# Optimization experiments

Measured on AMD Instinct MI355X. Metric: run time of the kernel, lower is better.

## Reference

```python
import jax, jax.numpy as jnp
import numpy as np

N_NODES = 20000
N_EDGES = 160000
N_CONFIG = 1000
OP_SIZE = 120
OP_FEATURE = 140
CONFIG_FEATURE = 24
HID = 256
EMB = 128


def _mynorm(x, axis):
    # InstanceNorm1d (affine=False): biased var, eps=1e-5, normalized over `axis`
    m = jnp.mean(x, axis=axis, keepdims=True)
    v = jnp.var(x, axis=axis, keepdims=True)
    return (x - m) / jnp.sqrt(v + 1e-5)


def _gelu(x):
    return jax.nn.gelu(x, approximate=False)


def _segment_softmax(e, seg, num):
    m = jax.ops.segment_max(e, seg, num_segments=num)
    ex = jnp.exp(e - m[seg])
    s = jax.ops.segment_sum(ex, seg, num_segments=num)
    return ex / (s[seg] + 1e-16)


def setup_inputs() -> dict:
    key = jax.random.key(0)
    ks = jax.random.split(key, 24)
    d = {}
    d['node_feat'] = jax.random.normal(ks[0], (N_NODES, OP_FEATURE), jnp.float32)
    d['config_feat'] = jax.random.normal(ks[1], (N_CONFIG, CONFIG_FEATURE), jnp.float32)
    d['node_feat_mean'] = jax.random.normal(ks[2], (OP_FEATURE,), jnp.float32)
    d['node_feat_std'] = jax.random.uniform(ks[3], (OP_FEATURE,), jnp.float32)
    d['config_feat_mean'] = jax.random.normal(ks[4], (CONFIG_FEATURE,), jnp.float32)
    d['config_feat_std'] = jax.random.uniform(ks[5], (CONFIG_FEATURE,), jnp.float32)
    d['embed_table'] = jax.random.normal(ks[6], (OP_SIZE, EMB), jnp.float32)
    d['early_W1'] = jax.random.normal(ks[7], (EMB + OP_FEATURE, HID), jnp.float32) * 0.05
    d['early_W2'] = jax.random.normal(ks[8], (HID, HID), jnp.float32) * 0.05
    d['gat_Wl'] = jax.random.normal(ks[9], (4, HID, HID), jnp.float32) * 0.05
    d['gat_bl'] = jax.random.normal(ks[10], (4, HID), jnp.float32) * 0.05
    d['gat_Wr'] = jax.random.normal(ks[11], (4, HID, HID), jnp.float32) * 0.05
    d['gat_br'] = jax.random.normal(ks[12], (4, HID), jnp.float32) * 0.05
    d['gat_att'] = jax.random.normal(ks[13], (4, HID), jnp.float32) * 0.05
    d['gat_bias'] = jax.random.normal(ks[14], (4, HID), jnp.float32) * 0.05
    d['late_W1'] = jax.random.normal(ks[15], (HID + CONFIG_FEATURE, HID), jnp.float32) * 0.05
    d['late_W2'] = jax.random.normal(ks[16], (HID, HID // 2), jnp.float32) * 0.05
    d['pred_W'] = jax.random.normal(ks[17], (HID // 2, 1), jnp.float32) * 0.05
    d['pred_b'] = jax.random.normal(ks[18], (1,), jnp.float32) * 0.05
    d['node_opcode'] = jax.random.randint(ks[19], (N_NODES,), 0, OP_SIZE, jnp.int64)
    d['edge_index'] = jax.random.randint(ks[20], (2, N_EDGES), 0, N_NODES, jnp.int64)
    return d


def reference(node_feat, config_feat, node_feat_mean, node_feat_std,
              config_feat_mean, config_feat_std, embed_table,
              early_W1, early_W2, gat_Wl, gat_bl, gat_Wr, gat_br,
              gat_att, gat_bias, late_W1, late_W2, pred_W, pred_b,
              node_opcode, edge_index):
    N = node_feat.shape[0]
    # embedding with max_norm=1: renormalize looked-up rows to L2 norm <= 1
    emb = embed_table[node_opcode]
    nrm = jnp.sqrt(jnp.sum(emb * emb, axis=-1, keepdims=True))
    emb = emb * jnp.minimum(1.0, 1.0 / (nrm + 1e-7))
    feat = (node_feat - node_feat_mean) / (node_feat_std + 1e-4)
    x = jnp.concatenate([emb, feat], axis=-1)  # [N, 268]
    # early MLP (norm over node axis per channel)
    x = _gelu(_mynorm(x @ early_W1, 0))
    x = _gelu(_mynorm(x @ early_W2, 0))
    # add self loops (PyG GATv2Conv default)
    loop = jnp.arange(N, dtype=edge_index.dtype)
    src = jnp.concatenate([edge_index[0], loop])  # message source j
    dst = jnp.concatenate([edge_index[1], loop])  # message target i
    for i in range(4):
        xl = x @ gat_Wl[i] + gat_bl[i]
        xr = x @ gat_Wr[i] + gat_br[i]
        h = xl[src] + xr[dst]                      # [E+N, HID]
        e = jax.nn.leaky_relu(h, 0.2) @ gat_att[i]  # [E+N]
        alpha = _segment_softmax(e, dst, N)
        out = jax.ops.segment_sum(alpha[:, None] * xl[src], dst, num_segments=N)
        out = out + gat_bias[i]
        x = _gelu(_mynorm(out, 0))
    pool = jnp.mean(x, axis=0) + jnp.max(x, axis=0)  # [HID]
    cf = (config_feat - config_feat_mean) / (config_feat_std + 1e-4)
    C = cf.shape[0]
    x_late = jnp.concatenate([cf, jnp.broadcast_to(pool, (C, pool.shape[0]))], axis=1)
    h = _gelu(_mynorm(x_late @ late_W1, 0))  # 2D MyNorm1d normalizes over batch axis
    h = _gelu(_mynorm(h @ late_W2, 0))
    runtime = (h @ pred_W + pred_b)[:, 0]
    return runtime
```

## Files before the change

### kernel.cpp

```cpp
#include <hip/hip_runtime.h>
#include <math.h>

#define N_NODES 20000
#define N_EDGES 160000
#define N_CFG   1000
#define OP_FEAT 140
#define CFG_FEAT 24
#define HID     256
#define EMB     128
#define E_TOT   (N_EDGES + N_NODES)
#define K288    288
#define MPAD    20096
#define NW      512

typedef __attribute__((ext_vector_type(8))) short short8v;
typedef __attribute__((ext_vector_type(4))) float f32x4;

__device__ __forceinline__ short f2bf(float f) {
  unsigned u = __float_as_uint(f);
  unsigned r = (u + 0x7FFFu + ((u >> 16) & 1u)) >> 16;
  return (short)r;
}
__device__ __forceinline__ float bf2f(short s) {
  return __uint_as_float(((unsigned)(unsigned short)s) << 16);
}
__device__ __forceinline__ float gelu_f(float x) {
  return 0.5f * x * (1.0f + erff(x * 0.70710678118654752f));
}

#define GLOAD_LDS(gptr, lptr) __builtin_amdgcn_global_load_lds( \
    (const __attribute__((address_space(1))) void*)(gptr),      \
    (__attribute__((address_space(3))) void*)(lptr), 16, 0, 0)

__global__ void prep_weights(
    const float* __restrict__ eW1, const float* __restrict__ eW2,
    const float* __restrict__ lW1, const float* __restrict__ lW2,
    const float* __restrict__ Wl, const float* __restrict__ Wr,
    const float* __restrict__ bl, const float* __restrict__ br,
    short* __restrict__ W1t, short* __restrict__ W2t,
    short* __restrict__ lW1t, short* __restrict__ lW2t,
    short* __restrict__ Wlrt, float* __restrict__ blr)
{
  int i = blockIdx.x * 256 + threadIdx.x;
  const int s1 = HID * K288;
  const int s2 = HID * HID;
  const int s3 = HID * K288;
  const int s4 = 128 * HID;
  const int s5 = 4 * NW * HID;
  const int s6 = 4 * NW;
  if (i < s1) { int n = i / K288, k = i % K288;
    W1t[i] = (k < EMB + OP_FEAT) ? f2bf(eW1[(size_t)k * HID + n]) : (short)0; return; }
  i -= s1;
  if (i < s2) { int n = i >> 8, k = i & 255;
    W2t[i] = f2bf(eW2[(size_t)k * HID + n]); return; }
  i -= s2;
  if (i < s3) { int n = i / K288, k = i % K288;
    lW1t[i] = (k < CFG_FEAT + HID) ? f2bf(lW1[(size_t)k * HID + n]) : (short)0; return; }
  i -= s3;
  if (i < s4) { int n = i >> 8, k = i & 255;
    lW2t[i] = f2bf(lW2[(size_t)k * 128 + n]); return; }
  i -= s4;
  if (i < s5) { int l = i >> 17, rem = i & 131071, n = rem >> 8, k = rem & 255;
    float v = (n < HID) ? Wl[(size_t)l * HID * HID + (size_t)k * HID + n]
                        : Wr[(size_t)l * HID * HID + (size_t)k * HID + (n - HID)];
    Wlrt[i] = f2bf(v); return; }
  i -= s5;
  if (i < s6) { int l = i >> 9, j = i & 511;
    blr[i] = (j < HID) ? bl[l * HID + j] : br[l * HID + j - HID]; }
}

__global__ __launch_bounds__(256) void prep_kernel(
    const float* __restrict__ node_feat, const float* __restrict__ nf_mean,
    const float* __restrict__ nf_std, const float* __restrict__ emb_table,
    const int* __restrict__ opcode, short* __restrict__ x268b)
{
  int wave = threadIdx.x >> 6;
  int lane = threadIdx.x & 63;
  int row = blockIdx.x * 4 + wave;
  if (row >= N_NODES) return;
  int op = opcode[row];
  float t0 = emb_table[op * EMB + lane];
  float t1 = emb_table[op * EMB + 64 + lane];
  float ss = t0 * t0 + t1 * t1;
  #pragma unroll
  for (int off = 32; off; off >>= 1) ss += __shfl_xor(ss, off);
  float sc = fminf(1.0f, 1.0f / (sqrtf(ss) + 1e-7f));
  short* dst = x268b + (size_t)row * K288;
  dst[lane] = f2bf(t0 * sc);
  dst[64 + lane] = f2bf(t1 * sc);
  for (int k = lane; k < OP_FEAT; k += 64)
    dst[EMB + k] = f2bf((node_feat[(size_t)row * OP_FEAT + k] - nf_mean[k]) / (nf_std[k] + 1e-4f));
  if (lane < K288 - EMB - OP_FEAT) dst[EMB + OP_FEAT + lane] = 0;
}

template<int BM, int BN>
__global__ __launch_bounds__(256) void gemm_mfma(
    const short* __restrict__ A, const short* __restrict__ Wt,
    const float* __restrict__ bias, float* __restrict__ C,
    short* __restrict__ Cb, float* __restrict__ stats,
    int M, int N, int Kpad)
{
  constexpr int MI = (BM == 128) ? 4 : 2;
  constexpr int NI = (BN == 128) ? 4 : 2;
  __shared__ __align__(16) short As[2][4][BM][8];
  __shared__ __align__(16) short Bs[2][4][BN][8];
  int tid = threadIdx.x;
  int wave = tid >> 6, lane = tid & 63;
  int bm = blockIdx.x * BM, bn = blockIdx.y * BN;
  int wr = (BM == 128) ? (wave >> 1) * 64 : (wave >> 1) * 32;
  int wc = (BM == 128) ? (wave & 1) * 64 : (wave & 1) * 32;
  int g = lane >> 4, r16 = lane & 15;
  f32x4 acc[MI][NI] = {};
  int nt = Kpad >> 5;

  auto STAGE = [&](int t, int b) {
    int k0 = t * 32;
    if constexpr (BM == 128) {
      #pragma unroll
      for (int s2 = 0; s2 < 2; s2++) {
        int s = wave * 2 + s2;
        int sg = s >> 1, r0 = (s & 1) * 64;
        GLOAD_LDS(A  + (size_t)(bm + r0 + lane) * Kpad + k0 + sg * 8, &As[b][sg][r0][0]);
        GLOAD_LDS(Wt + (size_t)(bn + r0 + lane) * Kpad + k0 + sg * 8, &Bs[b][sg][r0][0]);
      }
    } else {
      GLOAD_LDS(A  + (size_t)(bm + lane) * Kpad + k0 + wave * 8, &As[b][wave][0][0]);
      GLOAD_LDS(Wt + (size_t)(bn + lane) * Kpad + k0 + wave * 8, &Bs[b][wave][0][0]);
    }
  };

  STAGE(0, 0);
  for (int t = 0; t < nt; t++) {
    int b = t & 1;
    __syncthreads();
    if (t + 1 < nt) STAGE(t + 1, b ^ 1);
    short8v af[MI], bfv[NI];
    #pragma unroll
    for (int mi = 0; mi < MI; mi++)
      af[mi] = *(const short8v*)&As[b][g][wr + mi * 16 + r16][0];
    #pragma unroll
    for (int ni = 0; ni < NI; ni++)
      bfv[ni] = *(const short8v*)&Bs[b][g][wc + ni * 16 + r16][0];
    #pragma unroll
    for (int mi = 0; mi < MI; mi++)
      #pragma unroll
      for (int ni = 0; ni < NI; ni++)
        acc[mi][ni] = __builtin_amdgcn_mfma_f32_16x16x32_bf16(af[mi], bfv[ni], acc[mi][ni], 0, 0, 0);
  }

  int rg = lane >> 4;
  #pragma unroll
  for (int ni = 0; ni < NI; ni++) {
    int gc = bn + wc + ni * 16 + r16;
    float bv = bias ? bias[gc] : 0.f;
    float s = 0.f, sq = 0.f;
    #pragma unroll
    for (int mi = 0; mi < MI; mi++) {
      #pragma unroll
      for (int r = 0; r < 4; r++) {
        int gr = bm + wr + mi * 16 + rg * 4 + r;
        if (gr < M) {
          float v = acc[mi][ni][r] + bv;
          if (C)  C[(size_t)gr * N + gc] = v;
          if (Cb) Cb[(size_t)gr * N + gc] = f2bf(v);
          s += v; sq += v * v;
        }
      }
    }
    if (stats) {
      s  += __shfl_xor(s, 16);  sq += __shfl_xor(sq, 16);
      s  += __shfl_xor(s, 32);  sq += __shfl_xor(sq, 32);
      if (rg == 0) { atomicAdd(&stats[gc], s); atomicAdd(&stats[N + gc], sq); }
    }
  }
}

__global__ void colstats(const float* __restrict__ X, int M, int C,
                         float* __restrict__ stats)
{
  int c = threadIdx.x;
  int r0 = blockIdx.x * 64;
  int r1 = min(r0 + 64, M);
  float s = 0.f, sq = 0.f;
  for (int r = r0; r < r1; r++) {
    float v = X[(size_t)r * C + c];
    s += v; sq += v * v;
  }
  atomicAdd(&stats[c], s);
  atomicAdd(&stats[C + c], sq);
}

__global__ void norm_gelu_col(const float* __restrict__ X, short* __restrict__ Yb,
                              int M, int C, const float* __restrict__ stats,
                              float* __restrict__ psum, unsigned* __restrict__ pmax)
{
  int c = threadIdx.x;
  int r0 = blockIdx.x * 32, r1 = min(r0 + 32, M);
  float invM = 1.0f / (float)M;
  float mean = stats[c] * invM;
  float var = stats[C + c] * invM - mean * mean;
  float inv = rsqrtf(var + 1e-5f);
  float s = 0.f, mx = -INFINITY;
  for (int r = r0; r < r1; r++) {
    float y = gelu_f((X[(size_t)r * C + c] - mean) * inv);
    Yb[(size_t)r * C + c] = f2bf(y);
    s += y; mx = fmaxf(mx, y);
  }
  if (psum) {
    unsigned b = __float_as_uint(mx);
    unsigned enc = (b & 0x80000000u) ? ~b : (b | 0x80000000u);
    atomicAdd(&psum[c], s);
    atomicMax(&pmax[c], enc);
  }
}

__global__ void edge_count(const int* __restrict__ ei, int* __restrict__ counts) {
  int e = blockIdx.x * blockDim.x + threadIdx.x;
  if (e >= E_TOT) return;
  int dst = (e < N_EDGES) ? ei[N_EDGES + e] : (e - N_EDGES);
  atomicAdd(&counts[dst], 1);
}

__global__ __launch_bounds__(1024) void scan_kernel(const int* __restrict__ counts,
                                                    int* __restrict__ indptr)
{
  __shared__ int sh[1024];
  int t = threadIdx.x;
  const int chunk = (N_NODES + 1023) / 1024;
  int start = t * chunk, end = min(start + chunk, N_NODES);
  int sum = 0;
  for (int i = start; i < end; i++) sum += counts[i];
  sh[t] = sum;
  __syncthreads();
  for (int off = 1; off < 1024; off <<= 1) {
    int v = (t >= off) ? sh[t - off] : 0;
    __syncthreads();
    sh[t] += v;
    __syncthreads();
  }
  int run = (t > 0) ? sh[t - 1] : 0;
  for (int i = start; i < end; i++) { indptr[i] = run; run += counts[i]; }
  if (t == 1023) indptr[N_NODES] = run;
}

__global__ void edge_fill(const int* __restrict__ ei, const int* __restrict__ indptr,
                          int* __restrict__ cursor, int* __restrict__ col)
{
  int e = blockIdx.x * blockDim.x + threadIdx.x;
  if (e >= E_TOT) return;
  int src, dst;
  if (e < N_EDGES) { src = ei[e]; dst = ei[N_EDGES + e]; }
  else             { src = dst = e - N_EDGES; }
  int pos = indptr[dst] + atomicAdd(&cursor[dst], 1);
  col[pos] = src;
}

__global__ __launch_bounds__(256) void gat_agg(
    const short* __restrict__ xlr,
    const int* __restrict__ indptr, const int* __restrict__ col,
    const float* __restrict__ att, const float* __restrict__ bias,
    float* __restrict__ out)
{
  int wave = threadIdx.x >> 6, lane = threadIdx.x & 63;
  int node = blockIdx.x * 4 + wave;
  if (node >= N_NODES) return;
  float attc[4], xri[4], o[4] = {0, 0, 0, 0};
  {
    short4 xr4 = *(const short4*)(xlr + (size_t)node * NW + HID + lane * 4);
    #pragma unroll
    for (int k = 0; k < 4; k++) {
      attc[k] = att[lane * 4 + k];
      xri[k] = bf2f(((short*)&xr4)[k]);
    }
  }
  float m = -INFINITY, s = 0.f;
  int e0 = indptr[node], e1 = indptr[node + 1];
  for (int e = e0; e < e1; e += 4) {
    float p[4];
    float xlj[4][4];
    #pragma unroll
    for (int b = 0; b < 4; b++) {
      bool valid = (e + b) < e1;
      int j = col[valid ? e + b : e0];
      short4 xl4 = *(const short4*)(xlr + (size_t)j * NW + lane * 4);
      float pp = 0.f;
      #pragma unroll
      for (int k = 0; k < 4; k++) {
        xlj[b][k] = bf2f(((short*)&xl4)[k]);
        float h = xlj[b][k] + xri[k];
        float lr = h > 0.f ? h : 0.2f * h;
        pp += lr * attc[k];
      }
      p[b] = valid ? pp : -INFINITY;
    }
    #pragma unroll
    for (int off = 32; off; off >>= 1) {
      #pragma unroll
      for (int b = 0; b < 4; b++) p[b] += __shfl_xor(p[b], off);
    }
    float mn = fmaxf(m, fmaxf(fmaxf(p[0], p[1]), fmaxf(p[2], p[3])));
    float scale = __expf(m - mn);
    float w[4];
    #pragma unroll
    for (int b = 0; b < 4; b++) w[b] = __expf(p[b] - mn);
    s = s * scale + w[0] + w[1] + w[2] + w[3];
    #pragma unroll
    for (int k = 0; k < 4; k++)
      o[k] = o[k] * scale + w[0] * xlj[0][k] + w[1] * xlj[1][k]
                          + w[2] * xlj[2][k] + w[3] * xlj[3][k];
    m = mn;
  }
  float inv = 1.0f / (s + 1e-16f);
  f32x4 ov;
  #pragma unroll
  for (int k = 0; k < 4; k++) ov[k] = o[k] * inv + bias[lane * 4 + k];
  *(f32x4*)(out + (size_t)node * HID + lane * 4) = ov;
}

__device__ __forceinline__ float fdec(unsigned u) {
  unsigned b = (u & 0x80000000u) ? (u & 0x7FFFFFFFu) : ~u;
  return __uint_as_float(b);
}

__global__ void build_xlate(const float* __restrict__ cfg, const float* __restrict__ cmean,
                            const float* __restrict__ cstd, const float* __restrict__ psum,
                            const unsigned* __restrict__ pmax, short* __restrict__ xlateb)
{
  int i = blockIdx.x * blockDim.x + threadIdx.x;
  if (i >= N_CFG * K288) return;
  int r = i / K288, c = i % K288;
  float v;
  if (c < CFG_FEAT) v = (cfg[r * CFG_FEAT + c] - cmean[c]) / (cstd[c] + 1e-4f);
  else if (c < CFG_FEAT + HID) {
    int p = c - CFG_FEAT;
    v = psum[p] * (1.0f / N_NODES) + fdec(pmax[p]);
  } else v = 0.f;
  xlateb[i] = f2bf(v);
}

__global__ __launch_bounds__(64) void pred_kernel(
    const float* __restrict__ h2, const float* __restrict__ stats,
    const float* __restrict__ W, const float* __restrict__ b,
    float* __restrict__ out)
{
  int r = blockIdx.x, lane = threadIdx.x;
  const float invM = 1.0f / (float)N_CFG;
  float v = 0.f;
  #pragma unroll
  for (int t = 0; t < 2; t++) {
    int c = lane + 64 * t;
    float mean = stats[c] * invM;
    float var = stats[128 + c] * invM - mean * mean;
    float y = gelu_f((h2[(size_t)r * 128 + c] - mean) * rsqrtf(var + 1e-5f));
    v += y * W[c];
  }
  #pragma unroll
  for (int off = 32; off; off >>= 1) v += __shfl_xor(v, off);
  if (lane == 0) out[r] = v + b[0];
}

extern "C" void kernel_launch(void* const* d_in, const int* in_sizes, int n_in,
                              void* d_out, int out_size, void* d_ws, size_t ws_size,
                              hipStream_t stream)
{
  const float* node_feat   = (const float*)d_in[0];
  const float* config_feat = (const float*)d_in[1];
  const float* nf_mean     = (const float*)d_in[2];
  const float* nf_std      = (const float*)d_in[3];
  const float* cf_mean     = (const float*)d_in[4];
  const float* cf_std      = (const float*)d_in[5];
  const float* emb_table   = (const float*)d_in[6];
  const float* early_W1    = (const float*)d_in[7];
  const float* early_W2    = (const float*)d_in[8];
  const float* gat_Wl      = (const float*)d_in[9];
  const float* gat_bl      = (const float*)d_in[10];
  const float* gat_Wr      = (const float*)d_in[11];
  const float* gat_br      = (const float*)d_in[12];
  const float* gat_att     = (const float*)d_in[13];
  const float* gat_bias    = (const float*)d_in[14];
  const float* late_W1     = (const float*)d_in[15];
  const float* late_W2     = (const float*)d_in[16];
  const float* pred_W      = (const float*)d_in[17];
  const float* pred_b      = (const float*)d_in[18];
  const int*   node_opcode = (const int*)d_in[19];
  const int*   edge_index  = (const int*)d_in[20];
  float* out = (float*)d_out;
  (void)in_sizes; (void)n_in; (void)out_size; (void)ws_size;

  char* ws = (char*)d_ws;
  size_t off = 0;
  auto alloc = [&](size_t bytes) -> void* {
    void* p = ws + off;
    off += (bytes + 255) & ~255ull;
    return p;
  };
  short* x268b = (short*)alloc((size_t)MPAD * K288 * 2);
  float* bufB  = (float*)alloc((size_t)N_NODES * HID * 4);
  short* bufAb = (short*)alloc((size_t)MPAD * HID * 2);
  short* xlr   = (short*)alloc((size_t)N_NODES * NW * 2);
  int* indptr  = (int*)alloc((N_NODES + 1) * 4);
  int* colidx  = (int*)alloc((size_t)E_TOT * 4);
  short* xlateb = (short*)alloc((size_t)1024 * K288 * 2);
  float* h1    = (float*)alloc((size_t)N_CFG * HID * 4);
  short* h1b   = (short*)alloc((size_t)1024 * HID * 2);
  float* h2    = (float*)alloc((size_t)N_CFG * 128 * 4);
  short* W1t   = (short*)alloc((size_t)HID * K288 * 2);
  short* W2t   = (short*)alloc((size_t)HID * HID * 2);
  short* Wlrt  = (short*)alloc((size_t)4 * NW * HID * 2);
  float* blr   = (float*)alloc(4 * NW * 4);
  short* lW1t  = (short*)alloc((size_t)HID * K288 * 2);
  short* lW2t  = (short*)alloc((size_t)128 * HID * 2);

  float* zbase = (float*)alloc((8 * 1024 + 512 + 2 * N_NODES) * 4);
  float* stats8 = zbase;
  float* psum   = zbase + 8192;
  unsigned* pmax = (unsigned*)(zbase + 8192 + 256);
  int* counts   = (int*)(zbase + 8192 + 512);
  int* cursor   = counts + N_NODES;
  const size_t zbytes = (8 * 1024 + 512 + 2 * N_NODES) * 4;
  auto slot = [&](int s) { return stats8 + s * 1024; };

  auto run_gemm = [&](int BM, const short* A, const short* Wt, const float* bias, float* C,
                      short* Cb, float* stats, int M, int N, int Kpad) {
    if (BM == 128) {
      dim3 grid((M + 127) / 128, N / 128);
      hipLaunchKernelGGL((gemm_mfma<128, 128>), grid, dim3(256), 0, stream,
                         A, Wt, bias, C, Cb, stats, M, N, Kpad);
    } else {
      dim3 grid((M + 63) / 64, N / 64);
      hipLaunchKernelGGL((gemm_mfma<64, 64>), grid, dim3(256), 0, stream,
                         A, Wt, bias, C, Cb, stats, M, N, Kpad);
    }
  };
  auto run_norm = [&](const float* X, short* Yb, int M, int C, float* stats,
                      float* ps, unsigned* pm) {
    hipLaunchKernelGGL(norm_gelu_col, dim3((M + 31) / 32), dim3(C), 0, stream,
                       X, Yb, M, C, stats, ps, pm);
  };

  hipMemsetAsync(zbase, 0, zbytes, stream);

  {
    int total = HID * K288 + HID * HID + HID * K288 + 128 * HID + 4 * NW * HID + 4 * NW;
    hipLaunchKernelGGL(prep_weights, dim3((total + 255) / 256), dim3(256), 0, stream,
                       early_W1, early_W2, late_W1, late_W2, gat_Wl, gat_Wr, gat_bl, gat_br,
                       W1t, W2t, lW1t, lW2t, Wlrt, blr);
  }

  hipLaunchKernelGGL(edge_count, dim3((E_TOT + 255) / 256), dim3(256), 0, stream,
                     edge_index, counts);
  hipLaunchKernelGGL(scan_kernel, dim3(1), dim3(1024), 0, stream, counts, indptr);
  hipLaunchKernelGGL(edge_fill, dim3((E_TOT + 255) / 256), dim3(256), 0, stream,
                     edge_index, indptr, cursor, colidx);

  hipLaunchKernelGGL(prep_kernel, dim3((N_NODES + 3) / 4), dim3(256), 0, stream,
                     node_feat, nf_mean, nf_std, emb_table, node_opcode, x268b);
  run_gemm(64, x268b, W1t, nullptr, bufB, nullptr, slot(0), N_NODES, HID, K288);
  run_norm(bufB, bufAb, N_NODES, HID, slot(0), nullptr, nullptr);
  run_gemm(64, bufAb, W2t, nullptr, bufB, nullptr, slot(1), N_NODES, HID, HID);
  run_norm(bufB, bufAb, N_NODES, HID, slot(1), nullptr, nullptr);

  for (int l = 0; l < 4; l++) {
    run_gemm(128, bufAb, Wlrt + (size_t)l * NW * HID, blr + l * NW, nullptr, xlr, nullptr,
             N_NODES, NW, HID);
    hipLaunchKernelGGL(gat_agg, dim3((N_NODES + 3) / 4), dim3(256), 0, stream,
                       xlr, indptr, colidx, gat_att + l * HID, gat_bias + l * HID, bufB);
    hipLaunchKernelGGL(colstats, dim3((N_NODES + 63) / 64), dim3(HID), 0, stream,
                       bufB, N_NODES, HID, slot(2 + l));
    run_norm(bufB, bufAb, N_NODES, HID, slot(2 + l),
             (l == 3) ? psum : nullptr, (l == 3) ? pmax : nullptr);
  }

  hipLaunchKernelGGL(build_xlate, dim3((N_CFG * K288 + 255) / 256), dim3(256), 0, stream,
                     config_feat, cf_mean, cf_std, psum, pmax, xlateb);
  run_gemm(64, xlateb, lW1t, nullptr, h1, nullptr, slot(6), N_CFG, HID, K288);
  run_norm(h1, h1b, N_CFG, HID, slot(6), nullptr, nullptr);
  run_gemm(64, h1b, lW2t, nullptr, h2, nullptr, slot(7), N_CFG, 128, HID);
  hipLaunchKernelGGL(pred_kernel, dim3(N_CFG), dim3(64), 0, stream,
                     h2, slot(7), pred_W, pred_b, out);
}
```

Measured before the change: 560.7 us.

## Fuse column statistics into GAT aggregation and process two nodes per wave

Removes the separate colstats pass by accumulating per-column sum and sum-of-squares in shared memory inside gat_agg and flushing them with one global atomic per column per block. Each wave now handles two destination nodes, with 32 lanes per node doing 8-wide bf16 loads, which halves the shuffle reduction depth and widens memory accesses. The two half-waves iterate to the larger of the two degrees, so uneven degrees waste some work. Shared-memory atomics add contention in exchange for skipping a full re-read of the 20000x256 fp32 output.

Result: slower. 726.2 us (+29.5%).

```diff
diff --git a/kernel.cpp b/kernel.cpp
--- a/kernel.cpp
+++ b/kernel.cpp
@@ -175,21 +175,6 @@
   }
 }
 
-__global__ void colstats(const float* __restrict__ X, int M, int C,
-                         float* __restrict__ stats)
-{
-  int c = threadIdx.x;
-  int r0 = blockIdx.x * 64;
-  int r1 = min(r0 + 64, M);
-  float s = 0.f, sq = 0.f;
-  for (int r = r0; r < r1; r++) {
-    float v = X[(size_t)r * C + c];
-    s += v; sq += v * v;
-  }
-  atomicAdd(&stats[c], s);
-  atomicAdd(&stats[C + c], sq);
-}
-
 __global__ void norm_gelu_col(const float* __restrict__ X, short* __restrict__ Yb,
                               int M, int C, const float* __restrict__ stats,
                               float* __restrict__ psum, unsigned* __restrict__ pmax)
@@ -259,34 +244,43 @@
     const short* __restrict__ xlr,
     const int* __restrict__ indptr, const int* __restrict__ col,
     const float* __restrict__ att, const float* __restrict__ bias,
-    float* __restrict__ out)
-{
-  int wave = threadIdx.x >> 6, lane = threadIdx.x & 63;
-  int node = blockIdx.x * 4 + wave;
-  if (node >= N_NODES) return;
-  float attc[4], xri[4], o[4] = {0, 0, 0, 0};
+    float* __restrict__ out, float* __restrict__ stats)
+{
+  __shared__ float sums[HID];
+  __shared__ float sqs[HID];
+  int tid = threadIdx.x;
+  if (tid < HID) { sums[tid] = 0.f; sqs[tid] = 0.f; }
+  __syncthreads();
+  int wave = tid >> 6, lane = tid & 63;
+  int hw = lane >> 5, ln = lane & 31;
+  int node = blockIdx.x * 8 + wave * 2 + hw;
+  float attc[8], xri[8], o[8] = {0, 0, 0, 0, 0, 0, 0, 0};
   {
-    short4 xr4 = *(const short4*)(xlr + (size_t)node * NW + HID + lane * 4);
-    #pragma unroll
-    for (int k = 0; k < 4; k++) {
-      attc[k] = att[lane * 4 + k];
-      xri[k] = bf2f(((short*)&xr4)[k]);
-    }
-  }
+    short8v xr8 = *(const short8v*)(xlr + (size_t)node * NW + HID + ln * 8);
+    #pragma unroll
+    for (int k = 0; k < 8; k++) {
+      attc[k] = att[ln * 8 + k];
+      xri[k] = bf2f(xr8[k]);
+    }
+  }
+  int e0 = indptr[node], e1 = indptr[node + 1];
+  int deg = e1 - e0;
+  int dother = __shfl_xor(deg, 32);
+  int iters = (max(deg, dother) + 3) >> 2;
   float m = -INFINITY, s = 0.f;
-  int e0 = indptr[node], e1 = indptr[node + 1];
-  for (int e = e0; e < e1; e += 4) {
+  for (int it = 0; it < iters; it++) {
+    int base = e0 + it * 4;
     float p[4];
-    float xlj[4][4];
+    float xlj[4][8];
     #pragma unroll
     for (int b = 0; b < 4; b++) {
-      bool valid = (e + b) < e1;
-      int j = col[valid ? e + b : e0];
-      short4 xl4 = *(const short4*)(xlr + (size_t)j * NW + lane * 4);
+      bool valid = (base + b) < e1;
+      int j = col[valid ? base + b : e0];
+      short8v v8 = *(const short8v*)(xlr + (size_t)j * NW + ln * 8);
       float pp = 0.f;
       #pragma unroll
-      for (int k = 0; k < 4; k++) {
-        xlj[b][k] = bf2f(((short*)&xl4)[k]);
+      for (int k = 0; k < 8; k++) {
+        xlj[b][k] = bf2f(v8[k]);
         float h = xlj[b][k] + xri[k];
         float lr = h > 0.f ? h : 0.2f * h;
         pp += lr * attc[k];
@@ -294,7 +288,7 @@
       p[b] = valid ? pp : -INFINITY;
     }
     #pragma unroll
-    for (int off = 32; off; off >>= 1) {
+    for (int off = 16; off; off >>= 1) {
       #pragma unroll
       for (int b = 0; b < 4; b++) p[b] += __shfl_xor(p[b], off);
     }
@@ -305,16 +299,27 @@
     for (int b = 0; b < 4; b++) w[b] = __expf(p[b] - mn);
     s = s * scale + w[0] + w[1] + w[2] + w[3];
     #pragma unroll
-    for (int k = 0; k < 4; k++)
+    for (int k = 0; k < 8; k++)
       o[k] = o[k] * scale + w[0] * xlj[0][k] + w[1] * xlj[1][k]
                           + w[2] * xlj[2][k] + w[3] * xlj[3][k];
     m = mn;
   }
   float inv = 1.0f / (s + 1e-16f);
-  f32x4 ov;
+  f32x4 ov0, ov1;
   #pragma unroll
-  for (int k = 0; k < 4; k++) ov[k] = o[k] * inv + bias[lane * 4 + k];
-  *(f32x4*)(out + (size_t)node * HID + lane * 4) = ov;
+  for (int k = 0; k < 8; k++) {
+    float v = o[k] * inv + bias[ln * 8 + k];
+    if (k < 4) ov0[k] = v; else ov1[k - 4] = v;
+    atomicAdd(&sums[ln * 8 + k], v);
+    atomicAdd(&sqs[ln * 8 + k], v * v);
+  }
+  *(f32x4*)(out + (size_t)node * HID + ln * 8) = ov0;
+  *(f32x4*)(out + (size_t)node * HID + ln * 8 + 4) = ov1;
+  __syncthreads();
+  if (tid < HID) {
+    atomicAdd(&stats[tid], sums[tid]);
+    atomicAdd(&stats[HID + tid], sqs[tid]);
+  }
 }
 
 __device__ __forceinline__ float fdec(unsigned u) {
@@ -463,10 +468,9 @@
   for (int l = 0; l < 4; l++) {
     run_gemm(128, bufAb, Wlrt + (size_t)l * NW * HID, blr + l * NW, nullptr, xlr, nullptr,
              N_NODES, NW, HID);
-    hipLaunchKernelGGL(gat_agg, dim3((N_NODES + 3) / 4), dim3(256), 0, stream,
-                       xlr, indptr, colidx, gat_att + l * HID, gat_bias + l * HID, bufB);
-    hipLaunchKernelGGL(colstats, dim3((N_NODES + 63) / 64), dim3(HID), 0, stream,
-                       bufB, N_NODES, HID, slot(2 + l));
+    hipLaunchKernelGGL(gat_agg, dim3(N_NODES / 8), dim3(256), 0, stream,
+                       xlr, indptr, colidx, gat_att + l * HID, gat_bias + l * HID,
+                       bufB, slot(2 + l));
     run_norm(bufB, bufAb, N_NODES, HID, slot(2 + l),
              (l == 3) ? psum : nullptr, (l == 3) ? pmax : nullptr);
   }
```
